# Performance work log

Hardware: AMD Instinct MI355X
Metric: run time of the kernel (lower is better)

The kernel has to match this reference:

```python
import jax, jax.numpy as jnp
import numpy as np

EMB = 1024
HEADS = 16
HEAD_DIM = EMB // HEADS


def setup_inputs() -> dict:
    key = jax.random.key(0)
    ks = jax.random.split(key, 7)
    B, Sq, Sk = 4, 1024, 1024
    dp_emb = jax.random.normal(ks[0], (B, Sq, EMB), dtype=jnp.float32)
    dp_mask = jnp.ones((B, 1, 1, Sq), dtype=jnp.float32)
    K = jax.random.normal(ks[1], (B, HEADS, Sk, HEAD_DIM), dtype=jnp.float32)
    V = jax.random.normal(ks[2], (B, HEADS, Sk, HEAD_DIM), dtype=jnp.float32)
    M = jax.random.normal(ks[3], (B, HEADS, Sq, Sk), dtype=jnp.float32)
    # query Linear params (key/value Linears in the torch module are unused)
    Wq = jax.random.normal(ks[4], (EMB, EMB), dtype=jnp.float32) / np.sqrt(EMB)
    bq = jax.random.normal(ks[5], (EMB,), dtype=jnp.float32) * 0.01
    return {"dp_emb": dp_emb, "dp_mask": dp_mask, "K": K, "V": V, "M": M, "Wq": Wq, "bq": bq}


def reference(dp_emb, dp_mask, K, V, M, Wq, bq):
    B, Sq, E = dp_emb.shape
    H, d = HEADS, HEAD_DIM
    # query projection: nn.Linear -> x @ W.T + b
    q = dp_emb @ Wq.T + bq                                  # [B,Sq,E]
    q = q.reshape(B, Sq, H, d).transpose(0, 2, 1, 3)        # [B,H,Sq,d]
    scores = jnp.einsum('bhqd,bhkd->bhqk', q, K) / np.sqrt(d).astype(jnp.float32)
    scores = scores - M                                      # additive mask (subtraction)
    probs = jax.nn.softmax(scores, axis=-1)                  # [B,H,Sq,Sk]
    # (probs.T * dp_mask).T == probs * dp_mask reshaped to mask the query axis
    probs = probs * jnp.swapaxes(dp_mask, -1, -2)            # dp_mask [B,1,1,Sq] -> [B,1,Sq,1]
    target_score = jnp.sum(jnp.max(probs, axis=2), axis=1)   # [B,Sk]
    # dropout omitted (eval/inference semantics)
    ctx = jnp.einsum('bhqk,bhkd->bhqd', probs, V)            # [B,H,Sq,d]
    ctx = ctx.transpose(0, 2, 1, 3).reshape(B, Sq, E)
    return ctx, target_score
```

## Files before the change

kernel.cpp:

```cpp
#include <hip/hip_runtime.h>

#define B_ 4
#define H_ 16
#define SQ 1024
#define SK 1024
#define DHD 64
#define E_ 1024

typedef _Float16 half_t;
typedef __attribute__((ext_vector_type(8))) _Float16 half8;
typedef __attribute__((ext_vector_type(4))) _Float16 half4;
typedef __attribute__((ext_vector_type(4))) float f32x4;

static __device__ __forceinline__ f32x4 mfma16h(half8 a, half8 b, f32x4 c) {
  return __builtin_amdgcn_mfma_f32_16x16x32_f16(a, b, c, 0, 0, 0);
}

#define QW_BLOCKS 2560
__global__ __launch_bounds__(256) void prep_kernel(const float* __restrict__ emb,
                                                   const float* __restrict__ wq,
                                                   const float* __restrict__ K,
                                                   const float* __restrict__ V,
                                                   half_t* __restrict__ emb_h,
                                                   half_t* __restrict__ wq_h,
                                                   half_t* __restrict__ khn,
                                                   half_t* __restrict__ vt) {
  int bid = blockIdx.x, tid = threadIdx.x;
  if (bid < QW_BLOCKS) {
    int i = bid * 256 + tid;
    const float* src;
    half_t* dst;
    if (i < (B_ * SQ * E_ / 8)) {
      src = emb;
      dst = emb_h;
    } else {
      i -= B_ * SQ * E_ / 8;
      src = wq;
      dst = wq_h;
    }
    size_t off = (size_t)i * 8;
    f32x4 v0 = *(const f32x4*)(src + off);
    f32x4 v1 = *(const f32x4*)(src + off + 4);
    half8 h;
#pragma unroll
    for (int j = 0; j < 4; ++j) {
      h[j] = (half_t)v0[j];
      h[4 + j] = (half_t)v1[j];
    }
    *(half8*)(dst + off) = h;
    return;
  }
  bid -= QW_BLOCKS;
  int bh = bid >> 4, kt = bid & 15;
  const float* ks = K + ((size_t)bh * SK + kt * 64) * DHD;
  half_t* kd = khn + ((size_t)bh * SK + kt * 64) * DHD;
#pragma unroll
  for (int j = 0; j < 2; ++j) {
    int base = j * 2048 + tid * 8;
    f32x4 a = *(const f32x4*)(ks + base);
    f32x4 b = *(const f32x4*)(ks + base + 4);
    half8 h;
#pragma unroll
    for (int r = 0; r < 4; ++r) {
      h[r] = (half_t)(-a[r]);
      h[4 + r] = (half_t)(-b[r]);
    }
    *(half8*)(kd + base) = h;
  }
  __shared__ float tile[64][65];
  const float* vs = V + ((size_t)bh * SK + kt * 64) * DHD;
#pragma unroll
  for (int i = 0; i < 16; ++i) {
    int idx = i * 256 + tid;
    tile[idx >> 6][idx & 63] = vs[idx];
  }
  __syncthreads();
#pragma unroll
  for (int i = 0; i < 16; ++i) {
    int idx = i * 256 + tid;
    int d = idx >> 6, kk = idx & 63;
    vt[((size_t)bh * DHD + d) * SK + kt * 64 + kk] = (half_t)tile[kk][d];
  }
}

__global__ __launch_bounds__(256) void proj_kernel(const half_t* __restrict__ emb,
                                                   const half_t* __restrict__ wq,
                                                   const float* __restrict__ bq,
                                                   half_t* __restrict__ qh) {
  int bid = blockIdx.x;
  int xcd = bid & 7, jj = bid >> 3;
  int mt = xcd * 8 + (jj >> 4);
  int nt = jj & 15;
  int tid = threadIdx.x, wid = tid >> 6, lane = tid & 63;
  int lr = lane & 15, lg = lane >> 4;
  int m0 = mt * 64 + (wid >> 1) * 32;
  int n0 = nt * 64 + (wid & 1) * 32;
  f32x4 acc[2][2];
#pragma unroll
  for (int i = 0; i < 2; ++i)
#pragma unroll
    for (int j = 0; j < 2; ++j) acc[i][j] = (f32x4){0.f, 0.f, 0.f, 0.f};

  for (int kk = 0; kk < E_; kk += 32) {
    half8 a[2], b[2];
#pragma unroll
    for (int g = 0; g < 2; ++g) {
      a[g] = *(const half8*)(emb + (size_t)(m0 + g * 16 + lr) * E_ + kk + lg * 8);
      b[g] = *(const half8*)(wq + (size_t)(n0 + g * 16 + lr) * E_ + kk + lg * 8);
    }
#pragma unroll
    for (int i = 0; i < 2; ++i)
#pragma unroll
      for (int j = 0; j < 2; ++j) acc[i][j] = mfma16h(a[i], b[j], acc[i][j]);
  }
#pragma unroll
  for (int i = 0; i < 2; ++i)
#pragma unroll
    for (int j = 0; j < 2; ++j)
#pragma unroll
      for (int r = 0; r < 4; ++r) {
        int m = m0 + i * 16 + lg * 4 + r;
        int n = n0 + j * 16 + lr;
        float v = (acc[i][j][r] + bq[n]) * 0.125f;
        int b = m >> 10, sq = m & 1023, h = n >> 6, dd = n & 63;
        qh[((size_t)(b * H_ + h) * SQ + sq) * DHD + dd] = (half_t)v;
      }
}

__global__ __launch_bounds__(512, 4) void attn_kernel(const half_t* __restrict__ qh,
                                                      const half_t* __restrict__ khn,
                                                      const half_t* __restrict__ vt,
                                                      const float* __restrict__ M,
                                                      const float* __restrict__ dpm,
                                                      float* __restrict__ out,
                                                      float* __restrict__ pm) {
  __shared__ half_t panel[32][1032];
  __shared__ float rowscale[32];

  int bid = blockIdx.x;
  int x = bid & 7, j = bid >> 3;
  int bh = x * 8 + (j >> 5);
  int qt = j & 31;
  int q0 = qt << 5;
  int b = bh >> 4, h = bh & 15;

  int tid = threadIdx.x, wid = tid >> 6, lane = tid & 63;
  int lr = lane & 15, lg = lane >> 4;

  const half_t* qbase = qh + ((size_t)bh * SQ + q0) * DHD;
  half8 aq[2][2];
#pragma unroll
  for (int qg = 0; qg < 2; ++qg)
#pragma unroll
    for (int dh = 0; dh < 2; ++dh)
      aq[qg][dh] = *(const half8*)(qbase + (size_t)(qg * 16 + lr) * DHD + dh * 32 + lg * 8);

  int kc0 = wid * 128;
#pragma unroll
  for (int kt = 0; kt < 8; ++kt) {
    const half_t* kr = khn + ((size_t)bh * SK + kc0 + kt * 16 + lr) * DHD + lg * 8;
    half8 k0 = *(const half8*)(kr);
    half8 k1 = *(const half8*)(kr + 32);
#pragma unroll
    for (int qg = 0; qg < 2; ++qg) {
      f32x4 T = (f32x4){0.f, 0.f, 0.f, 0.f};
      T = mfma16h(k0, aq[qg][0], T);
      T = mfma16h(k1, aq[qg][1], T);
      half4 ph;
#pragma unroll
      for (int r = 0; r < 4; ++r) ph[r] = (half_t)__expf(-T[r]);
      *(half4*)&panel[qg * 16 + lr][kc0 + kt * 16 + lg * 4] = ph;
    }
  }
  __syncthreads();

  {
    int qr = tid >> 4;
    int sub = tid & 15;
    const float* mrow = M + ((size_t)bh * SQ + q0 + qr) * SK + sub * 4;
    half_t* prow = &panel[qr][sub * 4];
    float rsum = 0.f;
#pragma unroll
    for (int jj = 0; jj < 16; ++jj) {
      f32x4 m = *(const f32x4*)(mrow + jj * 64);
      half4 es = *(const half4*)(prow + jj * 64);
      half4 ph;
#pragma unroll
      for (int i = 0; i < 4; ++i) {
        float p = (float)es[i] * __expf(-m[i]);
        rsum += p;
        ph[i] = (half_t)p;
      }
      *(half4*)(prow + jj * 64) = ph;
    }
    rsum += __shfl_xor(rsum, 1);
    rsum += __shfl_xor(rsum, 2);
    rsum += __shfl_xor(rsum, 4);
    rsum += __shfl_xor(rsum, 8);
    if (sub == 0) rowscale[qr] = dpm[b * SQ + q0 + qr] / rsum;
  }
  __syncthreads();

  int qg = wid >> 2, d0 = (wid & 3) * 16;
  const half_t* vrow = vt + ((size_t)bh * DHD + d0 + lr) * SK;
  f32x4 acc = (f32x4){0.f, 0.f, 0.f, 0.f};
#pragma unroll 8
  for (int ks = 0; ks < SK; ks += 32) {
    half8 av = *(const half8*)(vrow + ks + lg * 8);
    half8 bp = *(const half8*)&panel[qg * 16 + lr][ks + lg * 8];
    acc = mfma16h(av, bp, acc);
  }
  float rs = rowscale[qg * 16 + lr];
  f32x4 res;
#pragma unroll
  for (int r = 0; r < 4; ++r) res[r] = acc[r] * rs;
  *(f32x4*)(out + ((size_t)b * SQ + q0 + qg * 16 + lr) * E_ + h * DHD + d0 + lg * 4) = res;

  {
    int c = tid * 2;
    float m0 = 0.f, m1 = 0.f;
#pragma unroll 8
    for (int r = 0; r < 32; ++r) {
      float w = rowscale[r];
      m0 = fmaxf(m0, (float)panel[r][c] * w);
      m1 = fmaxf(m1, (float)panel[r][c + 1] * w);
    }
    float* pmrow = pm + ((size_t)bh * 32 + qt) * SK + c;
    pmrow[0] = m0;
    pmrow[1] = m1;
  }
}

__global__ __launch_bounds__(256) void tscore_kernel(const float* __restrict__ pm,
                                                     float* __restrict__ out) {
  int bb = blockIdx.x;
  int b = bb >> 4, kq = bb & 15;
  int t = threadIdx.x;
  int kl = t & 63, hg = t >> 6;
  int k = kq * 64 + kl;
  float s = 0.f;
#pragma unroll
  for (int hh = hg * 4; hh < hg * 4 + 4; ++hh) {
    const float* p = pm + ((size_t)(b * H_ + hh) * 32) * SK + k;
    float mx = 0.f;
#pragma unroll
    for (int qt = 0; qt < 32; ++qt) mx = fmaxf(mx, p[(size_t)qt * SK]);
    s += mx;
  }
  __shared__ float red[4][64];
  red[hg][kl] = s;
  __syncthreads();
  if (t < 64)
    out[(size_t)B_ * SQ * E_ + b * SK + kq * 64 + t] =
        red[0][t] + red[1][t] + red[2][t] + red[3][t];
}

extern "C" void kernel_launch(void* const* d_in, const int* in_sizes, int n_in,
                              void* d_out, int out_size, void* d_ws, size_t ws_size,
                              hipStream_t stream) {
  const float* dp_emb = (const float*)d_in[0];
  const float* dp_mask = (const float*)d_in[1];
  const float* K = (const float*)d_in[2];
  const float* V = (const float*)d_in[3];
  const float* M = (const float*)d_in[4];
  const float* Wq = (const float*)d_in[5];
  const float* bq = (const float*)d_in[6];
  float* out = (float*)d_out;

  char* ws = (char*)d_ws;
  half_t* q_h = (half_t*)(ws);
  half_t* k_hn = (half_t*)(ws + (8ull << 20));
  half_t* vt_h = (half_t*)(ws + (16ull << 20));
  half_t* emb_h = (half_t*)(ws + (24ull << 20));
  half_t* wq_h = (half_t*)(ws + (32ull << 20));
  float* pm = (float*)(ws + (34ull << 20));

  prep_kernel<<<QW_BLOCKS + B_ * H_ * 16, 256, 0, stream>>>(dp_emb, Wq, K, V, emb_h, wq_h,
                                                            k_hn, vt_h);
  proj_kernel<<<1024, 256, 0, stream>>>(emb_h, wq_h, bq, q_h);
  attn_kernel<<<B_ * H_ * (SQ / 32), 512, 0, stream>>>(q_h, k_hn, vt_h, M, dp_mask, out, pm);
  tscore_kernel<<<64, 256, 0, stream>>>(pm, out);
}
```

Before: 212.6 us.

## Interleave QK^T exp with M-mask pass in chunks, prefetching M and using exp2

Splits the score computation into four key-column chunks. After each chunk, a lightweight LDS barrier runs the M-mask multiply and row-sum for that chunk while the next chunk's M values are prefetched into registers, overlapping global M loads with MFMA work. The 1/sqrt(d) scale is folded together with log2(e) into the Q projection so the kernel can use exp2f. The cost is more barriers (four instead of one) and extra register pressure from double-buffered M prefetch, under a launch bound of 4 blocks per CU.

```diff
diff --git a/kernel.cpp b/kernel.cpp
--- a/kernel.cpp
+++ b/kernel.cpp
@@ -14,6 +14,10 @@
 
 static __device__ __forceinline__ f32x4 mfma16h(half8 a, half8 b, f32x4 c) {
   return __builtin_amdgcn_mfma_f32_16x16x32_f16(a, b, c, 0, 0, 0);
+}
+static __device__ __forceinline__ void lds_barrier() {
+  asm volatile("s_waitcnt lgkmcnt(0)" ::: "memory");
+  __builtin_amdgcn_s_barrier();
 }
 
 #define QW_BLOCKS 2560
@@ -121,7 +125,7 @@
       for (int r = 0; r < 4; ++r) {
         int m = m0 + i * 16 + lg * 4 + r;
         int n = n0 + j * 16 + lr;
-        float v = (acc[i][j][r] + bq[n]) * 0.125f;
+        float v = (acc[i][j][r] + bq[n]) * 0.180336880f;
         int b = m >> 10, sq = m & 1023, h = n >> 6, dd = n & 63;
         qh[((size_t)(b * H_ + h) * SQ + sq) * DHD + dd] = (half_t)v;
       }
@@ -155,51 +159,61 @@
     for (int dh = 0; dh < 2; ++dh)
       aq[qg][dh] = *(const half8*)(qbase + (size_t)(qg * 16 + lr) * DHD + dh * 32 + lg * 8);
 
-  int kc0 = wid * 128;
-#pragma unroll
-  for (int kt = 0; kt < 8; ++kt) {
-    const half_t* kr = khn + ((size_t)bh * SK + kc0 + kt * 16 + lr) * DHD + lg * 8;
-    half8 k0 = *(const half8*)(kr);
-    half8 k1 = *(const half8*)(kr + 32);
-#pragma unroll
-    for (int qg = 0; qg < 2; ++qg) {
-      f32x4 T = (f32x4){0.f, 0.f, 0.f, 0.f};
-      T = mfma16h(k0, aq[qg][0], T);
-      T = mfma16h(k1, aq[qg][1], T);
+  int qr = wid * 4 + lg;
+  const float* mrow = M + ((size_t)bh * SQ + q0 + qr) * SK + lr * 4;
+  half_t* prow = &panel[qr][lr * 4];
+  float rsum = 0.f;
+
+  f32x4 st[2][4];
+#pragma unroll
+  for (int i = 0; i < 4; ++i) st[0][i] = *(const f32x4*)(mrow + i * 64);
+
+#pragma unroll
+  for (int c = 0; c < 4; ++c) {
+    int kc0 = c * 256 + wid * 32;
+#pragma unroll
+    for (int kt = 0; kt < 2; ++kt) {
+      const half_t* kr = khn + ((size_t)bh * SK + kc0 + kt * 16 + lr) * DHD + lg * 8;
+      half8 k0 = *(const half8*)(kr);
+      half8 k1 = *(const half8*)(kr + 32);
+#pragma unroll
+      for (int qg = 0; qg < 2; ++qg) {
+        f32x4 T = (f32x4){0.f, 0.f, 0.f, 0.f};
+        T = mfma16h(k0, aq[qg][0], T);
+        T = mfma16h(k1, aq[qg][1], T);
+        half4 ph;
+#pragma unroll
+        for (int r = 0; r < 4; ++r) ph[r] = (half_t)exp2f(-T[r]);
+        *(half4*)&panel[qg * 16 + lr][kc0 + kt * 16 + lg * 4] = ph;
+      }
+    }
+    if (c < 3) {
+#pragma unroll
+      for (int i = 0; i < 4; ++i)
+        st[(c + 1) & 1][i] = *(const f32x4*)(mrow + (c + 1) * 256 + i * 64);
+    }
+    lds_barrier();
+#pragma unroll
+    for (int i = 0; i < 4; ++i) {
+      f32x4 m = st[c & 1][i];
+      half4 es = *(const half4*)(prow + c * 256 + i * 64);
       half4 ph;
 #pragma unroll
-      for (int r = 0; r < 4; ++r) ph[r] = (half_t)__expf(-T[r]);
-      *(half4*)&panel[qg * 16 + lr][kc0 + kt * 16 + lg * 4] = ph;
-    }
-  }
-  __syncthreads();
-
-  {
-    int qr = tid >> 4;
-    int sub = tid & 15;
-    const float* mrow = M + ((size_t)bh * SQ + q0 + qr) * SK + sub * 4;
-    half_t* prow = &panel[qr][sub * 4];
-    float rsum = 0.f;
-#pragma unroll
-    for (int jj = 0; jj < 16; ++jj) {
-      f32x4 m = *(const f32x4*)(mrow + jj * 64);
-      half4 es = *(const half4*)(prow + jj * 64);
-      half4 ph;
-#pragma unroll
-      for (int i = 0; i < 4; ++i) {
-        float p = (float)es[i] * __expf(-m[i]);
+      for (int r = 0; r < 4; ++r) {
+        float p = (float)es[r] * __expf(-m[r]);
         rsum += p;
-        ph[i] = (half_t)p;
+        ph[r] = (half_t)p;
       }
-      *(half4*)(prow + jj * 64) = ph;
-    }
-    rsum += __shfl_xor(rsum, 1);
-    rsum += __shfl_xor(rsum, 2);
-    rsum += __shfl_xor(rsum, 4);
-    rsum += __shfl_xor(rsum, 8);
-    if (sub == 0) rowscale[qr] = dpm[b * SQ + q0 + qr] / rsum;
-  }
-  __syncthreads();
+      *(half4*)(prow + c * 256 + i * 64) = ph;
+    }
+  }
+
+  rsum += __shfl_xor(rsum, 1);
+  rsum += __shfl_xor(rsum, 2);
+  rsum += __shfl_xor(rsum, 4);
+  rsum += __shfl_xor(rsum, 8);
+  if (lr == 0) rowscale[qr] = dpm[b * SQ + q0 + qr] / rsum;
+  lds_barrier();
 
   int qg = wid >> 2, d0 = (wid & 3) * 16;
   const half_t* vrow = vt + ((size_t)bh * DHD + d0 + lr) * SK;
```

After: 207.4 us. 2.4% less time.

## Split warps between QK^T scoring and mask-exp loading to overlap memory with compute

Applied to the files above, without the earlier changes.

Half the warps compute the QK^T scores with exp2, with the log2e factor folded into the query scale. The other half stream the large M tensor and write exp(-M) into a second shared panel, so the M load runs concurrently with the MFMA work. The combine step then only multiplies the two shared panels. This doubles shared memory per block and lowers the launch-bounds occupancy hint from 4 to 2. It also adds an fp16 rounding of exp(-M), which risks overflow for strongly negative M.

```diff
diff --git a/kernel.cpp b/kernel.cpp
--- a/kernel.cpp
+++ b/kernel.cpp
@@ -121,13 +121,13 @@
       for (int r = 0; r < 4; ++r) {
         int m = m0 + i * 16 + lg * 4 + r;
         int n = n0 + j * 16 + lr;
-        float v = (acc[i][j][r] + bq[n]) * 0.125f;
+        float v = (acc[i][j][r] + bq[n]) * 0.180336880f;
         int b = m >> 10, sq = m & 1023, h = n >> 6, dd = n & 63;
         qh[((size_t)(b * H_ + h) * SQ + sq) * DHD + dd] = (half_t)v;
       }
 }
 
-__global__ __launch_bounds__(512, 4) void attn_kernel(const half_t* __restrict__ qh,
+__global__ __launch_bounds__(512, 2) void attn_kernel(const half_t* __restrict__ qh,
                                                       const half_t* __restrict__ khn,
                                                       const half_t* __restrict__ vt,
                                                       const float* __restrict__ M,
@@ -135,6 +135,7 @@
                                                       float* __restrict__ out,
                                                       float* __restrict__ pm) {
   __shared__ half_t panel[32][1032];
+  __shared__ half_t em[32][1032];
   __shared__ float rowscale[32];
 
   int bid = blockIdx.x;
@@ -147,51 +148,68 @@
   int tid = threadIdx.x, wid = tid >> 6, lane = tid & 63;
   int lr = lane & 15, lg = lane >> 4;
 
-  const half_t* qbase = qh + ((size_t)bh * SQ + q0) * DHD;
-  half8 aq[2][2];
-#pragma unroll
-  for (int qg = 0; qg < 2; ++qg)
-#pragma unroll
-    for (int dh = 0; dh < 2; ++dh)
-      aq[qg][dh] = *(const half8*)(qbase + (size_t)(qg * 16 + lr) * DHD + dh * 32 + lg * 8);
-
-  int kc0 = wid * 128;
-#pragma unroll
-  for (int kt = 0; kt < 8; ++kt) {
-    const half_t* kr = khn + ((size_t)bh * SK + kc0 + kt * 16 + lr) * DHD + lg * 8;
-    half8 k0 = *(const half8*)(kr);
-    half8 k1 = *(const half8*)(kr + 32);
-#pragma unroll
-    for (int qg = 0; qg < 2; ++qg) {
-      f32x4 T = (f32x4){0.f, 0.f, 0.f, 0.f};
-      T = mfma16h(k0, aq[qg][0], T);
-      T = mfma16h(k1, aq[qg][1], T);
+  if (wid < 4) {
+    const half_t* qbase = qh + ((size_t)bh * SQ + q0) * DHD;
+    half8 aq[2][2];
+#pragma unroll
+    for (int qg = 0; qg < 2; ++qg)
+#pragma unroll
+      for (int dh = 0; dh < 2; ++dh)
+        aq[qg][dh] =
+            *(const half8*)(qbase + (size_t)(qg * 16 + lr) * DHD + dh * 32 + lg * 8);
+    int kc0 = wid * 256;
+#pragma unroll
+    for (int kt = 0; kt < 16; ++kt) {
+      const half_t* kr = khn + ((size_t)bh * SK + kc0 + kt * 16 + lr) * DHD + lg * 8;
+      half8 k0 = *(const half8*)(kr);
+      half8 k1 = *(const half8*)(kr + 32);
+#pragma unroll
+      for (int qg = 0; qg < 2; ++qg) {
+        f32x4 T = (f32x4){0.f, 0.f, 0.f, 0.f};
+        T = mfma16h(k0, aq[qg][0], T);
+        T = mfma16h(k1, aq[qg][1], T);
+        half4 ph;
+#pragma unroll
+        for (int r = 0; r < 4; ++r) ph[r] = (half_t)exp2f(-T[r]);
+        *(half4*)&panel[qg * 16 + lr][kc0 + kt * 16 + lg * 4] = ph;
+      }
+    }
+  } else {
+    int mt = (wid - 4) * 64 + lane;
+    int row = mt >> 3;
+    int cb = (mt & 7) * 4;
+    const float* mr = M + ((size_t)bh * SQ + q0 + row) * SK + cb;
+#pragma unroll
+    for (int hf = 0; hf < 2; ++hf) {
+      f32x4 mv[16];
+#pragma unroll
+      for (int i = 0; i < 16; ++i) mv[i] = *(const f32x4*)(mr + (hf * 16 + i) * 32);
+#pragma unroll
+      for (int i = 0; i < 16; ++i) {
+        half4 e;
+#pragma unroll
+        for (int r = 0; r < 4; ++r) e[r] = (half_t)__expf(-mv[i][r]);
+        *(half4*)&em[row][cb + (hf * 16 + i) * 32] = e;
+      }
+    }
+  }
+  __syncthreads();
+
+  {
+    int qr = tid >> 4, sub = tid & 15;
+    float rsum = 0.f;
+#pragma unroll
+    for (int jj = 0; jj < 16; ++jj) {
+      half4 es = *(const half4*)&panel[qr][sub * 4 + jj * 64];
+      half4 ev = *(const half4*)&em[qr][sub * 4 + jj * 64];
       half4 ph;
 #pragma unroll
-      for (int r = 0; r < 4; ++r) ph[r] = (half_t)__expf(-T[r]);
-      *(half4*)&panel[qg * 16 + lr][kc0 + kt * 16 + lg * 4] = ph;
-    }
-  }
-  __syncthreads();
-
-  {
-    int qr = tid >> 4;
-    int sub = tid & 15;
-    const float* mrow = M + ((size_t)bh * SQ + q0 + qr) * SK + sub * 4;
-    half_t* prow = &panel[qr][sub * 4];
-    float rsum = 0.f;
-#pragma unroll
-    for (int jj = 0; jj < 16; ++jj) {
-      f32x4 m = *(const f32x4*)(mrow + jj * 64);
-      half4 es = *(const half4*)(prow + jj * 64);
-      half4 ph;
-#pragma unroll
-      for (int i = 0; i < 4; ++i) {
-        float p = (float)es[i] * __expf(-m[i]);
+      for (int r = 0; r < 4; ++r) {
+        float p = (float)es[r] * (float)ev[r];
         rsum += p;
-        ph[i] = (half_t)p;
+        ph[r] = (half_t)p;
       }
-      *(half4*)(prow + jj * 64) = ph;
+      *(half4*)&panel[qr][sub * 4 + jj * 64] = ph;
     }
     rsum += __shfl_xor(rsum, 1);
     rsum += __shfl_xor(rsum, 2);
```

After: 238.6 us (median of 2 runs). +12.2%, slower.

## Halve attention query tile, prefetch mask into LDS and fuse exp via exp2

Applied to the files above, without the earlier changes.

Reduces the attention block's query tile from 32 to 16 rows. The M tile is loaded first and staged as scaled fp16 in the LDS panel. QK^T and the mask are then combined into a single exp2 per element, with the log2e factor folded into the Q projection scale, and row sums are reduced through shuffles plus a small cross-wave buffer. Half the waves do the PV MFMA while the other half compute column maxima, the LDS footprint is halved, and occupancy bounds are raised. In exchange, K/V are reread twice as often, the partial-max buffer doubles, and rounding M to fp16 adds precision loss.

```diff
diff --git a/kernel.cpp b/kernel.cpp
--- a/kernel.cpp
+++ b/kernel.cpp
@@ -6,6 +6,7 @@
 #define SK 1024
 #define DHD 64
 #define E_ 1024
+#define LOG2E 1.44269504f
 
 typedef _Float16 half_t;
 typedef __attribute__((ext_vector_type(8))) _Float16 half8;
@@ -121,113 +122,112 @@
       for (int r = 0; r < 4; ++r) {
         int m = m0 + i * 16 + lg * 4 + r;
         int n = n0 + j * 16 + lr;
-        float v = (acc[i][j][r] + bq[n]) * 0.125f;
+        float v = (acc[i][j][r] + bq[n]) * (0.125f * LOG2E);
         int b = m >> 10, sq = m & 1023, h = n >> 6, dd = n & 63;
         qh[((size_t)(b * H_ + h) * SQ + sq) * DHD + dd] = (half_t)v;
       }
 }
 
-__global__ __launch_bounds__(512, 4) void attn_kernel(const half_t* __restrict__ qh,
+__global__ __launch_bounds__(512, 6) void attn_kernel(const half_t* __restrict__ qh,
                                                       const half_t* __restrict__ khn,
                                                       const half_t* __restrict__ vt,
                                                       const float* __restrict__ M,
                                                       const float* __restrict__ dpm,
                                                       float* __restrict__ out,
                                                       float* __restrict__ pm) {
-  __shared__ half_t panel[32][1032];
-  __shared__ float rowscale[32];
+  __shared__ half_t panel[16][1032];
+  __shared__ float wred[8][16];
+  __shared__ float rowscale[16];
 
   int bid = blockIdx.x;
   int x = bid & 7, j = bid >> 3;
-  int bh = x * 8 + (j >> 5);
-  int qt = j & 31;
-  int q0 = qt << 5;
+  int bh = x * 8 + (j >> 6);
+  int qt = j & 63;
+  int q0 = qt << 4;
   int b = bh >> 4, h = bh & 15;
 
   int tid = threadIdx.x, wid = tid >> 6, lane = tid & 63;
   int lr = lane & 15, lg = lane >> 4;
 
-  const half_t* qbase = qh + ((size_t)bh * SQ + q0) * DHD;
-  half8 aq[2][2];
-#pragma unroll
-  for (int qg = 0; qg < 2; ++qg)
-#pragma unroll
-    for (int dh = 0; dh < 2; ++dh)
-      aq[qg][dh] = *(const half8*)(qbase + (size_t)(qg * 16 + lr) * DHD + dh * 32 + lg * 8);
-
-  int kc0 = wid * 128;
-#pragma unroll
-  for (int kt = 0; kt < 8; ++kt) {
-    const half_t* kr = khn + ((size_t)bh * SK + kc0 + kt * 16 + lr) * DHD + lg * 8;
-    half8 k0 = *(const half8*)(kr);
-    half8 k1 = *(const half8*)(kr + 32);
-#pragma unroll
-    for (int qg = 0; qg < 2; ++qg) {
+  {
+    int row = tid >> 5, cb = (tid & 31) * 4;
+    const float* mr = M + ((size_t)bh * SQ + q0 + row) * SK + cb;
+    f32x4 mv[8];
+#pragma unroll
+    for (int jj = 0; jj < 8; ++jj) mv[jj] = *(const f32x4*)(mr + jj * 128);
+#pragma unroll
+    for (int jj = 0; jj < 8; ++jj) {
+      half4 e;
+#pragma unroll
+      for (int r = 0; r < 4; ++r) e[r] = (half_t)(mv[jj][r] * LOG2E);
+      *(half4*)&panel[row][cb + jj * 128] = e;
+    }
+  }
+  __syncthreads();
+
+  float rsum = 0.f;
+  {
+    const half_t* qbase = qh + ((size_t)bh * SQ + q0) * DHD;
+    half8 aq0 = *(const half8*)(qbase + (size_t)lr * DHD + lg * 8);
+    half8 aq1 = *(const half8*)(qbase + (size_t)lr * DHD + 32 + lg * 8);
+    int kc0 = wid * 128;
+#pragma unroll
+    for (int kt = 0; kt < 8; ++kt) {
+      const half_t* kr = khn + ((size_t)bh * SK + kc0 + kt * 16 + lr) * DHD + lg * 8;
+      half8 k0 = *(const half8*)(kr);
+      half8 k1 = *(const half8*)(kr + 32);
       f32x4 T = (f32x4){0.f, 0.f, 0.f, 0.f};
-      T = mfma16h(k0, aq[qg][0], T);
-      T = mfma16h(k1, aq[qg][1], T);
+      T = mfma16h(k0, aq0, T);
+      T = mfma16h(k1, aq1, T);
+      half4 ml = *(const half4*)&panel[lr][kc0 + kt * 16 + lg * 4];
       half4 ph;
 #pragma unroll
-      for (int r = 0; r < 4; ++r) ph[r] = (half_t)__expf(-T[r]);
-      *(half4*)&panel[qg * 16 + lr][kc0 + kt * 16 + lg * 4] = ph;
-    }
-  }
-  __syncthreads();
-
-  {
-    int qr = tid >> 4;
-    int sub = tid & 15;
-    const float* mrow = M + ((size_t)bh * SQ + q0 + qr) * SK + sub * 4;
-    half_t* prow = &panel[qr][sub * 4];
-    float rsum = 0.f;
-#pragma unroll
-    for (int jj = 0; jj < 16; ++jj) {
-      f32x4 m = *(const f32x4*)(mrow + jj * 64);
-      half4 es = *(const half4*)(prow + jj * 64);
-      half4 ph;
-#pragma unroll
-      for (int i = 0; i < 4; ++i) {
-        float p = (float)es[i] * __expf(-m[i]);
+      for (int r = 0; r < 4; ++r) {
+        float p = exp2f(-T[r] - (float)ml[r]);
         rsum += p;
-        ph[i] = (half_t)p;
+        ph[r] = (half_t)p;
       }
-      *(half4*)(prow + jj * 64) = ph;
-    }
-    rsum += __shfl_xor(rsum, 1);
-    rsum += __shfl_xor(rsum, 2);
-    rsum += __shfl_xor(rsum, 4);
-    rsum += __shfl_xor(rsum, 8);
-    if (sub == 0) rowscale[qr] = dpm[b * SQ + q0 + qr] / rsum;
-  }
-  __syncthreads();
-
-  int qg = wid >> 2, d0 = (wid & 3) * 16;
-  const half_t* vrow = vt + ((size_t)bh * DHD + d0 + lr) * SK;
-  f32x4 acc = (f32x4){0.f, 0.f, 0.f, 0.f};
+      *(half4*)&panel[lr][kc0 + kt * 16 + lg * 4] = ph;
+    }
+  }
+  rsum += __shfl_xor(rsum, 16);
+  rsum += __shfl_xor(rsum, 32);
+  if (lg == 0) wred[wid][lr] = rsum;
+  __syncthreads();
+  if (tid < 16) {
+    float s = 0.f;
+#pragma unroll
+    for (int w = 0; w < 8; ++w) s += wred[w][tid];
+    rowscale[tid] = dpm[b * SQ + q0 + tid] / s;
+  }
+  __syncthreads();
+
+  if (wid < 4) {
+    int d0 = wid * 16;
+    const half_t* vrow = vt + ((size_t)bh * DHD + d0 + lr) * SK;
+    f32x4 acc = (f32x4){0.f, 0.f, 0.f, 0.f};
 #pragma unroll 8
-  for (int ks = 0; ks < SK; ks += 32) {
-    half8 av = *(const half8*)(vrow + ks + lg * 8);
-    half8 bp = *(const half8*)&panel[qg * 16 + lr][ks + lg * 8];
-    acc = mfma16h(av, bp, acc);
-  }
-  float rs = rowscale[qg * 16 + lr];
-  f32x4 res;
-#pragma unroll
-  for (int r = 0; r < 4; ++r) res[r] = acc[r] * rs;
-  *(f32x4*)(out + ((size_t)b * SQ + q0 + qg * 16 + lr) * E_ + h * DHD + d0 + lg * 4) = res;
-
-  {
-    int c = tid * 2;
-    float m0 = 0.f, m1 = 0.f;
-#pragma unroll 8
-    for (int r = 0; r < 32; ++r) {
+    for (int ks = 0; ks < SK; ks += 32) {
+      half8 av = *(const half8*)(vrow + ks + lg * 8);
+      half8 bp = *(const half8*)&panel[lr][ks + lg * 8];
+      acc = mfma16h(av, bp, acc);
+    }
+    float rs = rowscale[lr];
+    f32x4 res;
+#pragma unroll
+    for (int r = 0; r < 4; ++r) res[r] = acc[r] * rs;
+    *(f32x4*)(out + ((size_t)b * SQ + q0 + lr) * E_ + h * DHD + d0 + lg * 4) = res;
+  } else {
+    int c0 = ((wid - 4) * 64 + lane) * 4;
+    f32x4 cm = (f32x4){0.f, 0.f, 0.f, 0.f};
+#pragma unroll
+    for (int r = 0; r < 16; ++r) {
+      half4 ph = *(const half4*)&panel[r][c0];
       float w = rowscale[r];
-      m0 = fmaxf(m0, (float)panel[r][c] * w);
-      m1 = fmaxf(m1, (float)panel[r][c + 1] * w);
-    }
-    float* pmrow = pm + ((size_t)bh * 32 + qt) * SK + c;
-    pmrow[0] = m0;
-    pmrow[1] = m1;
+#pragma unroll
+      for (int i = 0; i < 4; ++i) cm[i] = fmaxf(cm[i], (float)ph[i] * w);
+    }
+    *(f32x4*)(pm + ((size_t)bh * 64 + qt) * SK + c0) = cm;
   }
 }
 
@@ -241,10 +241,10 @@
   float s = 0.f;
 #pragma unroll
   for (int hh = hg * 4; hh < hg * 4 + 4; ++hh) {
-    const float* p = pm + ((size_t)(b * H_ + hh) * 32) * SK + k;
+    const float* p = pm + ((size_t)(b * H_ + hh) * 64) * SK + k;
     float mx = 0.f;
 #pragma unroll
-    for (int qt = 0; qt < 32; ++qt) mx = fmaxf(mx, p[(size_t)qt * SK]);
+    for (int qt = 0; qt < 64; ++qt) mx = fmaxf(mx, p[(size_t)qt * SK]);
     s += mx;
   }
   __shared__ float red[4][64];
@@ -278,6 +278,6 @@
   prep_kernel<<<QW_BLOCKS + B_ * H_ * 16, 256, 0, stream>>>(dp_emb, Wq, K, V, emb_h, wq_h,
                                                             k_hn, vt_h);
   proj_kernel<<<1024, 256, 0, stream>>>(emb_h, wq_h, bq, q_h);
-  attn_kernel<<<B_ * H_ * (SQ / 32), 512, 0, stream>>>(q_h, k_hn, vt_h, M, dp_mask, out, pm);
+  attn_kernel<<<B_ * H_ * (SQ / 16), 512, 0, stream>>>(q_h, k_hn, vt_h, M, dp_mask, out, pm);
   tscore_kernel<<<64, 256, 0, stream>>>(pm, out);
 }
```

Measured after the change: 235.1 us. 10.6% more time.
